# Optimization experiments

Measured on AMD Instinct MI355X. Metric: run time of the kernel, lower is better.

## Reference

```python
import jax, jax.numpy as jnp
import numpy as np

NUM_HEADS = 12
ROPE_THETA = 10000.0


def setup_inputs() -> dict:
    key = jax.random.key(0)
    ks = jax.random.split(key, 7)
    B, H, W, C = 4, 32, 32, 768
    hd = C // NUM_HEADS
    x = jax.random.normal(ks[0], (B, H, W, C), jnp.float32)
    qkv_w = jax.random.normal(ks[1], (3 * C, C), jnp.float32) * 0.02
    qkv_b = jax.random.normal(ks[2], (3 * C,), jnp.float32) * 0.02
    proj_w = jax.random.normal(ks[3], (C, C), jnp.float32) * 0.02
    proj_b = jax.random.normal(ks[4], (C,), jnp.float32) * 0.02
    rel_pos_h = jax.random.normal(ks[5], (2 * H - 1, hd), jnp.float32) * 0.02
    rel_pos_w = jax.random.normal(ks[6], (2 * W - 1, hd), jnp.float32) * 0.02
    return {"x": x, "qkv_w": qkv_w, "qkv_b": qkv_b, "proj_w": proj_w,
            "proj_b": proj_b, "rel_pos_h": rel_pos_h, "rel_pos_w": rel_pos_w}


def _axial_cis(hd, H, W, theta):
    # compute_axial_cis: frequencies over head_dim//4 bands per axis
    freqs = 1.0 / (theta ** (jnp.arange(0, hd, 4, dtype=jnp.float32)[: hd // 4] / hd))
    t = jnp.arange(H * W, dtype=jnp.float32)
    t_x = t % H          # end_x = input_size[0]
    t_y = jnp.floor(t / H)
    ang = jnp.concatenate([jnp.outer(t_x, freqs), jnp.outer(t_y, freqs)], axis=-1)  # (L, hd//2)
    return jax.lax.complex(jnp.cos(ang), jnp.sin(ang))


def _rope(x, cis):
    # x: (B, nh, L, hd); pairs of channels -> complex, rotate, back to real
    B, nh, L, hd = x.shape
    xr = x.reshape(B, nh, L, hd // 2, 2)
    xc = jax.lax.complex(xr[..., 0], xr[..., 1]) * cis[None, None]
    return jnp.stack([jnp.real(xc), jnp.imag(xc)], axis=-1).reshape(B, nh, L, hd)


def reference(x, qkv_w, qkv_b, proj_w, proj_b, rel_pos_h, rel_pos_w):
    B, H, W, C = x.shape
    nh = NUM_HEADS
    hd = C // nh
    L = H * W
    # fused QKV projection
    qkv = x.reshape(B, L, C) @ qkv_w.T + qkv_b              # (B, L, 3C)
    qkv = qkv.reshape(B, L, 3, nh, hd).transpose(2, 0, 3, 1, 4)
    q, k, v = qkv[0], qkv[1], qkv[2]                        # (B, nh, L, hd)
    # 2D axial RoPE on q, k
    cis = _axial_cis(hd, H, W, ROPE_THETA)
    q = _rope(q, cis)
    k = _rope(k, cis)
    # decomposed relative position bias (math of concat_rel_pos + SDPA w/ rescale)
    coords = jnp.arange(H)[:, None] - jnp.arange(W)[None, :] + (H - 1)  # (H, W), H == W
    Rh = rel_pos_h[coords]                                  # (q_h, k_h, hd)
    Rw = rel_pos_w[coords]                                  # (q_w, k_w, hd)
    rq = q.reshape(B, nh, H, W, hd)
    rel_h = jnp.einsum('bnhwc,hkc->bnhwk', rq, Rh)          # (B, nh, H, W, k_h)
    rel_w = jnp.einsum('bnhwc,wkc->bnhwk', rq, Rw)          # (B, nh, H, W, k_w)
    bias = (rel_h[..., :, None] + rel_w[..., None, :]).reshape(B, nh, L, L)
    scale = 1.0 / jnp.sqrt(jnp.float32(hd))
    scores = jnp.einsum('bnqc,bnkc->bnqk', q, k) * scale + bias
    attn = jax.nn.softmax(scores, axis=-1)
    out = jnp.einsum('bnqk,bnkc->bnqc', attn, v)            # (B, nh, L, hd)
    out = out.transpose(0, 2, 1, 3).reshape(B, H, W, C)
    return out @ proj_w.T + proj_b
```

## Files before the change

kernel.cpp:

```cpp
#include <hip/hip_runtime.h>
#include <hip/hip_bf16.h>
#include <stdint.h>

typedef __hip_bfloat16 bf16;
typedef __attribute__((ext_vector_type(8))) short bf16x8;
typedef __attribute__((ext_vector_type(4))) float f32x4;

#define MFMA16(a, b, c) __builtin_amdgcn_mfma_f32_16x16x32_bf16(a, b, c, 0, 0, 0)

__device__ __forceinline__ void gl_lds16(const void* g, void* l) {
  __builtin_amdgcn_global_load_lds(
      (const __attribute__((address_space(1))) uint32_t*)g,
      (__attribute__((address_space(3))) uint32_t*)l, 16, 0, 0);
}

struct alignas(8) bf16x4s { bf16 a, b, c, d; };

__device__ __forceinline__ void cast4(const float* __restrict__ src,
                                      bf16* __restrict__ dst, int i) {
  float4 v = ((const float4*)src)[i];
  bf16x4s o{__float2bfloat16(v.x), __float2bfloat16(v.y),
            __float2bfloat16(v.z), __float2bfloat16(v.w)};
  ((bf16x4s*)dst)[i] = o;
}

__global__ void k_prep(const float* __restrict__ x, const float* __restrict__ qkvw,
                       const float* __restrict__ projw, bf16* __restrict__ xb,
                       bf16* __restrict__ wqkvb, bf16* __restrict__ wprojb,
                       float* __restrict__ cosT, float* __restrict__ sinT) {
  const int bid = blockIdx.x, tid = threadIdx.x;
  if (bid < 3072) {
    cast4(x, xb, bid * 256 + tid);
  } else if (bid < 4800) {
    cast4(qkvw, wqkvb, (bid - 3072) * 256 + tid);
  } else if (bid < 5376) {
    cast4(projw, wprojb, (bid - 4800) * 256 + tid);
  } else {
    const int i = (bid - 5376) * 256 + tid;
    const int pos = i >> 5, p = i & 31;
    const int j = p & 15;
    const float t = (p < 16) ? (float)(pos & 31) : (float)(pos >> 5);
    const float f = powf(10000.0f, -(float)j / 16.0f);
    float sv, cv;
    sincosf(t * f, &sv, &cv);
    cosT[i] = cv;
    sinT[i] = sv;
  }
}

__device__ __forceinline__ void gemm128_loop(const bf16* __restrict__ A,
                                             const bf16* __restrict__ Bt,
                                             int m0, int n0, bf16* ldsA, bf16* ldsB,
                                             f32x4 acc[4][4]) {
  const int tid = threadIdx.x;
  const int lane = tid & 63, w = tid >> 6;
  const int wm = w >> 1, wn = w & 1;
  const int lr = lane & 15, lg = lane >> 4;
  const int off0 = w * 1024 + lane * 16;

  auto stage = [&](int kt, int buf) {
#pragma unroll
    for (int c = 0; c < 2; ++c) {
      const int o = c * 4096 + off0;
      const int row = o >> 6, colb = o & 63;
      gl_lds16((const char*)A + ((size_t)(m0 + row) * 768 + kt) * 2 + colb,
               (char*)ldsA + buf * 8192 + c * 4096 + w * 1024);
      gl_lds16((const char*)Bt + ((size_t)(n0 + row) * 768 + kt) * 2 + colb,
               (char*)ldsB + buf * 8192 + c * 4096 + w * 1024);
    }
  };

  stage(0, 0);
  __syncthreads();
  int cur = 0;
  for (int ki = 0; ki < 24; ++ki) {
    if (ki + 1 < 24) stage((ki + 1) * 32, cur ^ 1);
    const char* baseA = (const char*)ldsA + cur * 8192;
    const char* baseB = (const char*)ldsB + cur * 8192;
    bf16x8 af[4], bf_[4];
#pragma unroll
    for (int f = 0; f < 4; ++f) {
      af[f] = *(const bf16x8*)(baseA + (wm * 64 + f * 16 + lr) * 64 + lg * 16);
      bf_[f] = *(const bf16x8*)(baseB + (wn * 64 + f * 16 + lr) * 64 + lg * 16);
    }
#pragma unroll
    for (int fm = 0; fm < 4; ++fm)
#pragma unroll
      for (int fn = 0; fn < 4; ++fn)
        acc[fm][fn] = MFMA16(af[fm], bf_[fn], acc[fm][fn]);
    __syncthreads();
    cur ^= 1;
  }
}

__global__ __launch_bounds__(256, 3) void k_qkv(
    const bf16* __restrict__ xb, const bf16* __restrict__ wb, const float* __restrict__ qkvb,
    const float* __restrict__ cosT, const float* __restrict__ sinT,
    bf16* __restrict__ Qb, bf16* __restrict__ Kb, bf16* __restrict__ VbT) {
  __shared__ __align__(16) bf16 ldsA[2][128 * 32];
  __shared__ __align__(16) bf16 ldsB[2][128 * 32];
  const int m0 = (blockIdx.x & 31) * 128, n0 = (blockIdx.x >> 5) * 128;
  f32x4 acc[4][4] = {};
  gemm128_loop(xb, wb, m0, n0, &ldsA[0][0], &ldsB[0][0], acc);
  const int lane = threadIdx.x & 63, w = threadIdx.x >> 6;
  const int wm = w >> 1, wn = w & 1, lr = lane & 15, lg = lane >> 4;
#pragma unroll
  for (int fm = 0; fm < 4; ++fm) {
#pragma unroll
    for (int fn = 0; fn < 4; ++fn) {
      const int n = n0 + wn * 64 + fn * 16 + lr;
      const int sect = n / 768;
      const int cn = n - sect * 768;
      const int head = cn >> 6, d = cn & 63;
      const float bias = qkvb[n];
      const int p = d >> 1;
#pragma unroll
      for (int r = 0; r < 4; ++r) {
        const int m = m0 + wm * 64 + fm * 16 + lg * 4 + r;
        const int bb = m >> 10, pos = m & 1023;
        float val = acc[fm][fn][r] + bias;
        const float partner = __shfl_xor(val, 1);
        if (sect < 2) {
          const float cv = cosT[pos * 32 + p], sv = sinT[pos * 32 + p];
          val = (d & 1) ? (val * cv + partner * sv) : (val * cv - partner * sv);
        }
        const bf16 o = __float2bfloat16(val);
        const size_t base = (size_t)(bb * 12 + head) * 65536;
        if (sect == 0)      Qb[base + (size_t)pos * 64 + d] = o;
        else if (sect == 1) Kb[base + (size_t)pos * 64 + d] = o;
        else                VbT[base + (size_t)d * 1024 + pos] = o;
      }
    }
  }
}

__global__ __launch_bounds__(256) void k_relbias(
    const bf16* __restrict__ Qb, const float* __restrict__ relph,
    const float* __restrict__ relpw, float* __restrict__ relh,
    float* __restrict__ relw) {
  const int bid = blockIdx.x;
  const int bn = bid >> 4;
  const int rem = bid & 15;
  const bool isW = (rem >> 3) != 0;
  const int w = threadIdx.x >> 6;
  const int rc = (rem & 7) * 4 + w;
  const int lane = threadIdx.x & 63;
  const int lr = lane & 15, lg = lane >> 4;
  const float* __restrict__ relp = isW ? relpw : relph;

  bf16x8 af[2][2];
#pragma unroll
  for (int mb = 0; mb < 2; ++mb) {
    const int m = mb * 16 + lr;
    const int l = isW ? (m * 32 + rc) : (rc * 32 + m);
    const bf16* ap = Qb + (size_t)bn * 65536 + (size_t)l * 64 + lg * 8;
#pragma unroll
    for (int ks = 0; ks < 2; ++ks) af[mb][ks] = *(const bf16x8*)(ap + ks * 32);
  }
  bf16x8 bfr[2][2];
#pragma unroll
  for (int nb = 0; nb < 2; ++nb) {
    const int n = nb * 16 + lr;
    const float* bp = relp + (size_t)(31 + rc - n) * 64 + lg * 8;
#pragma unroll
    for (int ks = 0; ks < 2; ++ks) {
      const float4 f0 = *(const float4*)(bp + ks * 32);
      const float4 f1 = *(const float4*)(bp + ks * 32 + 4);
      bf16x8 t;
      ((bf16*)&t)[0] = __float2bfloat16(f0.x);
      ((bf16*)&t)[1] = __float2bfloat16(f0.y);
      ((bf16*)&t)[2] = __float2bfloat16(f0.z);
      ((bf16*)&t)[3] = __float2bfloat16(f0.w);
      ((bf16*)&t)[4] = __float2bfloat16(f1.x);
      ((bf16*)&t)[5] = __float2bfloat16(f1.y);
      ((bf16*)&t)[6] = __float2bfloat16(f1.z);
      ((bf16*)&t)[7] = __float2bfloat16(f1.w);
      bfr[nb][ks] = t;
    }
  }
  f32x4 acc[2][2] = {};
#pragma unroll
  for (int ks = 0; ks < 2; ++ks)
#pragma unroll
    for (int mb = 0; mb < 2; ++mb)
#pragma unroll
      for (int nb = 0; nb < 2; ++nb)
        acc[mb][nb] = MFMA16(af[mb][ks], bfr[nb][ks], acc[mb][nb]);
  float* __restrict__ dst = isW ? relw : relh;
#pragma unroll
  for (int mb = 0; mb < 2; ++mb)
#pragma unroll
    for (int nb = 0; nb < 2; ++nb)
#pragma unroll
      for (int r = 0; r < 4; ++r) {
        const int mo = mb * 16 + lg * 4 + r;
        const int n = nb * 16 + lr;
        const int l = isW ? (mo * 32 + rc) : (rc * 32 + mo);
        dst[(size_t)bn * 32768 + (size_t)l * 32 + n] = acc[mb][nb][r];
      }
}

__global__ __launch_bounds__(256, 3) void k_attn(
    const bf16* __restrict__ Qb, const bf16* __restrict__ Kb, const bf16* __restrict__ VbT,
    const float* __restrict__ relh, const float* __restrict__ relw, bf16* __restrict__ attno) {
  __shared__ __align__(16) bf16 Kt[2][64 * 64];
  __shared__ __align__(16) bf16 Vt[2][64 * 64];
  __shared__ __align__(16) float bH[64 * 33];
  __shared__ __align__(16) bf16 Pl[4][16 * 64];
  const int blk = blockIdx.x;
  const int bn = blk >> 4, qt = blk & 15;
  const int b = bn / 12, head = bn - b * 12;
  const int tid = threadIdx.x;
  const int lane = tid & 63, w = tid >> 6;
  const int lr = lane & 15, lg = lane >> 4;
  const size_t qkvbase = (size_t)bn * 65536;

  auto stageKV = [&](int kt, int buf) {
#pragma unroll
    for (int c = 0; c < 2; ++c) {
      const int off = c * 4096 + w * 1024 + lane * 16;
      const int row = off >> 7;
      const int loff = off ^ ((row & 7) << 4);
      gl_lds16((const char*)Kb + (qkvbase + (size_t)kt * 4096) * 2 + loff,
               (char*)Kt + buf * 8192 + c * 4096 + w * 1024);
      gl_lds16((const char*)VbT + (qkvbase + (size_t)row * 1024 + (size_t)kt * 64) * 2 + (loff & 127),
               (char*)Vt + buf * 8192 + c * 4096 + w * 1024);
    }
  };

  stageKV(0, 0);
  {
    const int r = tid >> 2, q8 = (tid & 3) * 8;
    const float* src = relh + (size_t)bn * 32768 + (size_t)(qt * 64 + r) * 32 + q8;
#pragma unroll
    for (int jj = 0; jj < 8; ++jj) bH[r * 33 + q8 + jj] = src[jj];
  }
  const int qrow_g = qt * 64 + w * 16 + lr;
  float bw[2][4];
  {
    const float* rw = relw + (size_t)bn * 32768 + (size_t)qrow_g * 32;
#pragma unroll
    for (int s1 = 0; s1 < 2; ++s1)
#pragma unroll
      for (int r = 0; r < 4; ++r) bw[s1][r] = rw[s1 * 16 + lg * 4 + r];
  }
  bf16x8 qf[2];
  {
    const char* qp = (const char*)(Qb + qkvbase + (size_t)qrow_g * 64);
    qf[0] = *(const bf16x8*)(qp + lg * 16);
    qf[1] = *(const bf16x8*)(qp + 64 + lg * 16);
  }
  f32x4 oacc[4] = {};
  float mrun = -1e30f, lrun = 0.0f;
  __syncthreads();
  int cur = 0;

  for (int kt = 0; kt < 16; ++kt) {
    if (kt + 1 < 16) stageKV(kt + 1, cur ^ 1);
    const char* Ktc = (const char*)Kt + cur * 8192;
    const char* Vtc = (const char*)Vt + cur * 8192;
    f32x4 sa[4];
    const int sw = (lr & 7) << 4;
#pragma unroll
    for (int s = 0; s < 4; ++s) {
      const int krow = s * 16 + lr;
      bf16x8 k0 = *(const bf16x8*)(Ktc + ((krow * 128 + lg * 16) ^ sw));
      bf16x8 k1 = *(const bf16x8*)(Ktc + ((krow * 128 + 64 + lg * 16) ^ sw));
      f32x4 z = {};
      z = MFMA16(k0, qf[0], z);
      z = MFMA16(k1, qf[1], z);
      sa[s] = z;
    }
    const float bh0 = bH[(w * 16 + lr) * 33 + 2 * kt];
    const float bh1 = bH[(w * 16 + lr) * 33 + 2 * kt + 1];
    float sc[16];
    float mt = -1e30f;
#pragma unroll
    for (int s = 0; s < 4; ++s) {
      const float bh = (s < 2) ? bh0 : bh1;
#pragma unroll
      for (int r = 0; r < 4; ++r) {
        const float v = sa[s][r] * 0.125f + bh + bw[s & 1][r];
        sc[s * 4 + r] = v;
        mt = fmaxf(mt, v);
      }
    }
    mt = fmaxf(mt, __shfl_xor(mt, 16));
    mt = fmaxf(mt, __shfl_xor(mt, 32));
    const float mnew = fmaxf(mrun, mt);
    const float alpha = __expf(mrun - mnew);
    float ps = 0.0f;
    short4 pk[4];
#pragma unroll
    for (int s = 0; s < 4; ++s) {
#pragma unroll
      for (int r = 0; r < 4; ++r) {
        const float p = __expf(sc[s * 4 + r] - mnew);
        ps += p;
        ((bf16*)&pk[s])[r] = __float2bfloat16(p);
      }
    }
    ps += __shfl_xor(ps, 16);
    ps += __shfl_xor(ps, 32);
    lrun = lrun * alpha + ps;
    mrun = mnew;
#pragma unroll
    for (int s = 0; s < 4; ++s) {
      int byteoff = (lr * 128 + s * 32 + lg * 8) ^ sw;
      *(short4*)((char*)Pl[w] + byteoff) = pk[s];
    }
#pragma unroll
    for (int r = 0; r < 4; ++r) {
      const float ar = __shfl(alpha, lg * 4 + r);
#pragma unroll
      for (int dblk = 0; dblk < 4; ++dblk) oacc[dblk][r] *= ar;
    }
    asm volatile("s_waitcnt lgkmcnt(0)" ::: "memory");
#pragma unroll
    for (int kh = 0; kh < 2; ++kh) {
      const int abyte = (lr * 128 + kh * 64 + lg * 16) ^ sw;
      const bf16x8 pa = *(const bf16x8*)((const char*)Pl[w] + abyte);
#pragma unroll
      for (int dblk = 0; dblk < 4; ++dblk) {
        const int vrow = dblk * 16 + lr;
        const bf16x8 vb = *(const bf16x8*)(Vtc + ((vrow * 128 + kh * 64 + lg * 16) ^ sw));
        oacc[dblk] = MFMA16(pa, vb, oacc[dblk]);
      }
    }
    __syncthreads();
    cur ^= 1;
  }
#pragma unroll
  for (int r = 0; r < 4; ++r) {
    const float lsum = __shfl(lrun, lg * 4 + r);
    const float inv = 1.0f / lsum;
    const int qg = qt * 64 + w * 16 + lg * 4 + r;
#pragma unroll
    for (int dblk = 0; dblk < 4; ++dblk) {
      attno[((size_t)b * 1024 + qg) * 768 + head * 64 + dblk * 16 + lr] =
          __float2bfloat16(oacc[dblk][r] * inv);
    }
  }
}

__global__ __launch_bounds__(256, 3) void k_proj(
    const bf16* __restrict__ attno, const bf16* __restrict__ pwb,
    const float* __restrict__ projb, float* __restrict__ out) {
  __shared__ __align__(16) bf16 ldsA[2][128 * 32];
  __shared__ __align__(16) bf16 ldsB[2][128 * 32];
  const int m0 = (blockIdx.x & 31) * 128, n0 = (blockIdx.x >> 5) * 128;
  f32x4 acc[4][4] = {};
  gemm128_loop(attno, pwb, m0, n0, &ldsA[0][0], &ldsB[0][0], acc);
  const int lane = threadIdx.x & 63, w = threadIdx.x >> 6;
  const int wm = w >> 1, wn = w & 1, lr = lane & 15, lg = lane >> 4;
#pragma unroll
  for (int fm = 0; fm < 4; ++fm) {
#pragma unroll
    for (int fn = 0; fn < 4; ++fn) {
      const int n = n0 + wn * 64 + fn * 16 + lr;
      const float bias = projb[n];
#pragma unroll
      for (int r = 0; r < 4; ++r) {
        const int m = m0 + wm * 64 + fm * 16 + lg * 4 + r;
        out[(size_t)m * 768 + n] = acc[fm][fn][r] + bias;
      }
    }
  }
}

extern "C" void kernel_launch(void* const* d_in, const int* in_sizes, int n_in,
                              void* d_out, int out_size, void* d_ws, size_t ws_size,
                              hipStream_t stream) {
  const float* x     = (const float*)d_in[0];
  const float* qkvw  = (const float*)d_in[1];
  const float* qkvb  = (const float*)d_in[2];
  const float* projw = (const float*)d_in[3];
  const float* projb = (const float*)d_in[4];
  const float* relph = (const float*)d_in[5];
  const float* relpw = (const float*)d_in[6];
  float* out = (float*)d_out;
  char* ws = (char*)d_ws;

  bf16*  xb     = (bf16*)(ws);
  bf16*  wqkvb  = (bf16*)(ws + 6291456);
  bf16*  wprojb = (bf16*)(ws + 9830400);
  float* cosT   = (float*)(ws + 11010048);
  float* sinT   = (float*)(ws + 11141120);
  bf16*  Qb     = (bf16*)(ws + 11272192);
  bf16*  Kb     = (bf16*)(ws + 17563648);
  bf16*  VbT    = (bf16*)(ws + 23855104);
  float* relh   = (float*)(ws + 30146560);
  float* relw   = (float*)(ws + 36438016);
  bf16*  attno  = (bf16*)(ws + 42729472);

  k_prep<<<5504, 256, 0, stream>>>(x, qkvw, projw, xb, wqkvb, wprojb, cosT, sinT);
  k_qkv<<<576, 256, 0, stream>>>(xb, wqkvb, qkvb, cosT, sinT, Qb, Kb, VbT);
  k_relbias<<<768, 256, 0, stream>>>(Qb, relph, relpw, relh, relw);
  k_attn<<<768, 256, 0, stream>>>(Qb, Kb, VbT, relh, relw, attno);
  k_proj<<<192, 256, 0, stream>>>(attno, wprojb, projb, out);
}
```

Measured before the change: 108.6 us.

## Use partial vmcnt waits for async LDS prefetch and remap attention block order

Replaces __syncthreads in the QKV GEMM loop and the attention KV loop with explicit s_waitcnt vmcnt(4)/lgkmcnt(0) plus raw s_barrier. The current buffer's global-to-LDS loads are waited on while the next tile's loads stay in flight, so prefetch overlaps compute and the barrier no longer drains all memory counters. Attention blocks are also remapped in an interleaved order (stride 96), which changes which heads and query tiles run concurrently and so changes cache locality. This relies on the exact count of outstanding loads per stage; if the compiler emits a different number of vector-memory ops, the waits may allow reads of incomplete data.

Result: no change. 108.6 us (+0.0%).

```diff
diff --git a/kernel.cpp b/kernel.cpp
--- a/kernel.cpp
+++ b/kernel.cpp
@@ -56,12 +56,11 @@
   const int lane = tid & 63, w = tid >> 6;
   const int wm = w >> 1, wn = w & 1;
   const int lr = lane & 15, lg = lane >> 4;
-  const int off0 = w * 1024 + lane * 16;
 
   auto stage = [&](int kt, int buf) {
 #pragma unroll
     for (int c = 0; c < 2; ++c) {
-      const int o = c * 4096 + off0;
+      const int o = c * 4096 + w * 1024 + lane * 16;
       const int row = o >> 6, colb = o & 63;
       gl_lds16((const char*)A + ((size_t)(m0 + row) * 768 + kt) * 2 + colb,
                (char*)ldsA + buf * 8192 + c * 4096 + w * 1024);
@@ -71,10 +70,15 @@
   };
 
   stage(0, 0);
-  __syncthreads();
   int cur = 0;
   for (int ki = 0; ki < 24; ++ki) {
-    if (ki + 1 < 24) stage((ki + 1) * 32, cur ^ 1);
+    if (ki + 1 < 24) {
+      stage((ki + 1) * 32, cur ^ 1);
+      asm volatile("s_waitcnt vmcnt(4)" ::: "memory");
+    } else {
+      asm volatile("s_waitcnt vmcnt(0)" ::: "memory");
+    }
+    __builtin_amdgcn_s_barrier();
     const char* baseA = (const char*)ldsA + cur * 8192;
     const char* baseB = (const char*)ldsB + cur * 8192;
     bf16x8 af[4], bf_[4];
@@ -88,7 +92,8 @@
 #pragma unroll
       for (int fn = 0; fn < 4; ++fn)
         acc[fm][fn] = MFMA16(af[fm], bf_[fn], acc[fm][fn]);
-    __syncthreads();
+    asm volatile("s_waitcnt lgkmcnt(0)" ::: "memory");
+    __builtin_amdgcn_s_barrier();
     cur ^= 1;
   }
 }
@@ -207,7 +212,8 @@
   __shared__ __align__(16) bf16 Vt[2][64 * 64];
   __shared__ __align__(16) float bH[64 * 33];
   __shared__ __align__(16) bf16 Pl[4][16 * 64];
-  const int blk = blockIdx.x;
+  const int blk0 = blockIdx.x;
+  const int blk = (blk0 & 7) * 96 + (blk0 >> 3);
   const int bn = blk >> 4, qt = blk & 15;
   const int b = bn / 12, head = bn - b * 12;
   const int tid = threadIdx.x;
@@ -252,11 +258,18 @@
   }
   f32x4 oacc[4] = {};
   float mrun = -1e30f, lrun = 0.0f;
-  __syncthreads();
+  asm volatile("s_waitcnt lgkmcnt(0)" ::: "memory");
+  __builtin_amdgcn_s_barrier();
   int cur = 0;
 
   for (int kt = 0; kt < 16; ++kt) {
-    if (kt + 1 < 16) stageKV(kt + 1, cur ^ 1);
+    if (kt + 1 < 16) {
+      stageKV(kt + 1, cur ^ 1);
+      asm volatile("s_waitcnt vmcnt(4)" ::: "memory");
+    } else {
+      asm volatile("s_waitcnt vmcnt(0)" ::: "memory");
+    }
+    __builtin_amdgcn_s_barrier();
     const char* Ktc = (const char*)Kt + cur * 8192;
     const char* Vtc = (const char*)Vt + cur * 8192;
     f32x4 sa[4];
@@ -327,7 +340,8 @@
         oacc[dblk] = MFMA16(pa, vb, oacc[dblk]);
       }
     }
-    __syncthreads();
+    asm volatile("s_waitcnt lgkmcnt(0)" ::: "memory");
+    __builtin_amdgcn_s_barrier();
     cur ^= 1;
   }
 #pragma unroll
```
